# Performance work log

Hardware: AMD Instinct MI355X
Metric: run time of the kernel (lower is better)

The kernel has to match this reference:

```python
import jax, jax.numpy as jnp
import numpy as np


def _leaky(x):
    return jnp.where(x >= 0, x, 0.01 * x)  # nn.LeakyReLU default slope


def _conv1x1(x, w):
    # x: [B, C, H, W], w: [O, C] (1x1 conv == per-pixel channel GEMM)
    return jnp.einsum('bchw,oc->bohw', x, w)


def setup_inputs() -> dict:
    key = jax.random.key(0)
    ks = jax.random.split(key, 12)

    def kaiming(k, o, c):  # kaiming_normal_ fan_out, relu gain, 1x1 kernel
        return jax.random.normal(k, (o, c), jnp.float32) * np.float32(np.sqrt(2.0 / o))

    lr_feature = jax.random.normal(ks[0], (1, 32, 256, 512), jnp.float32)
    hr_feature = jax.random.normal(ks[1], (1, 32, 512, 1024), jnp.float32)
    return {
        'lr_feature': lr_feature,
        'hr_feature': hr_feature,
        's1_w0': kaiming(ks[2], 128, 128),
        's1_w1': kaiming(ks[3], 64, 128),
        's1_w2': kaiming(ks[4], 32, 64),
        's1_w3': kaiming(ks[5], 16, 32),
        's1_w4': kaiming(ks[6], 8, 16),
        's1_w5': kaiming(ks[7], 1, 8),
        's2_w0': kaiming(ks[8], 3, 3),
        's2_w1': kaiming(ks[9], 2, 3),
        's2_w2': kaiming(ks[10], 1, 2),
        'fuse_w': jnp.ones((1, 2), jnp.float32),  # fuse weight initialized to 1
    }


def reference(lr_feature, hr_feature, s1_w0, s1_w1, s1_w2, s1_w3, s1_w4, s1_w5,
              s2_w0, s2_w1, s2_w2, fuse_w):
    scale = hr_feature.shape[-1] // lr_feature.shape[-1]  # static python int (=2, even)
    Hh, Wh = hr_feature.shape[-2], hr_feature.shape[-1]

    # nearest-neighbor upsample of lr_feature by `scale` (expand/view trick in torch)
    lr_up = jnp.repeat(jnp.repeat(lr_feature, scale, axis=2), scale, axis=3)

    # representation: [B, 128, Hh, Wh]
    rep = jnp.concatenate(
        [lr_up, hr_feature, lr_up * hr_feature, (lr_up - hr_feature) ** 2], axis=1)

    # similarity_measure1: 1x1-conv MLP chain 128->128->64->32->16->8->1
    o = _leaky(_conv1x1(rep, s1_w0))
    o = _leaky(_conv1x1(o, s1_w1))
    o = _leaky(_conv1x1(o, s1_w2))
    o = _leaky(_conv1x1(o, s1_w3))
    o = _conv1x1(o, s1_w4)
    weights1 = _conv1x1(o, s1_w5)  # [B, 1, Hh, Wh]

    # distance matrix (even-scale branch): 3 channels [dx, dy, norm]
    v = jnp.arange(-(scale // 2), scale // 2 + 1, dtype=jnp.float32)
    m = v.shape[0] // 2
    v = jnp.concatenate([v[:m], v[m + 1:]])  # drop center -> length `scale`
    d0 = jnp.broadcast_to(v[None, :], (scale, scale))
    dm = jnp.stack([d0, d0.T, jnp.sqrt(d0 ** 2 + d0.T ** 2)], axis=0)  # [3,s,s]
    dm = jnp.tile(dm, (1, Hh // scale, Wh // scale))[None]  # [1, 3, Hh, Wh]

    # similarity_measure2: 3->3->2->1
    w2 = _leaky(_conv1x1(dm, s2_w0))
    w2 = _leaky(_conv1x1(w2, s2_w1))
    weights2 = _conv1x1(w2, s2_w2)  # [1, 1, Hh, Wh]

    # fuse (weight forced non-negative via abs, as in forward's .data mutation)
    mapping = _conv1x1(jnp.concatenate([weights1, weights2], axis=1), jnp.abs(fuse_w))
    return mapping
```

## Files before the change

kernel.cpp:

```cpp
#include <hip/hip_runtime.h>

typedef short v8s __attribute__((ext_vector_type(8)));
typedef float v4f __attribute__((ext_vector_type(4)));
typedef unsigned v4u __attribute__((ext_vector_type(4)));

#define Wh   1024
#define Hh   512
#define HWh  (Wh * Hh)
#define Wlr  512
#define HWlr (Wlr * 256)
#define ITERS 4
#define NBLK  512

#define WFRAG_SHORTS (53 * 512)
#define LDS_FRAGS    48
#define LDS_BYTES    (LDS_FRAGS * 1024)

__device__ __forceinline__ unsigned short f2bf(float f) {
    union { float f; unsigned u; } v; v.f = f;
    unsigned r = v.u + 0x7FFFu + ((v.u >> 16) & 1u);
    return (unsigned short)(r >> 16);
}
__device__ __forceinline__ unsigned pk2(float a, float b) {
    unsigned r;
    asm("v_cvt_pk_bf16_f32 %0, %1, %2" : "=v"(r) : "v"(a), "v"(b));
    return r;
}
__device__ __forceinline__ float leaky(float x) { return fmaxf(x, 0.01f * x); }

__device__ __forceinline__ v8s relay(v4f e, v4f o) {
    v4u w;
    w[0] = pk2(leaky(e[0]), leaky(e[1]));
    w[1] = pk2(leaky(e[2]), leaky(e[3]));
    w[2] = pk2(leaky(o[0]), leaky(o[1]));
    w[3] = pk2(leaky(o[2]), leaky(o[3]));
    return __builtin_bit_cast(v8s, w);
}

__global__ void prep_kernel(const float* __restrict__ w0g, const float* __restrict__ w1g,
                            const float* __restrict__ w2g, const float* __restrict__ w3g,
                            unsigned short* __restrict__ ws)
{
    const int f = blockIdx.x;
    const int l = threadIdx.x;
    const int pp = l & 15, qq = l >> 4;
    unsigned short* dst = ws + f * 512 + l * 8;

    if (f < 32) {
        int mt = f >> 2, ks = f & 3;
        const float* src = w0g + (mt * 16 + pp) * 128 + ks * 32 + qq * 8;
#pragma unroll
        for (int j = 0; j < 8; ++j) dst[j] = f2bf(src[j]);
    } else if (f < 48) {
        int g = f - 32, mt = g >> 2, ks = g & 3;
        const float* srcrow = w1g + (mt * 16 + pp) * 128;
#pragma unroll
        for (int j = 0; j < 8; ++j)
            dst[j] = f2bf(srcrow[ks * 32 + ((j >> 2) << 4) + qq * 4 + (j & 3)]);
    } else if (f < 52) {
        int g = f - 48, mt = g >> 1, ks = g & 1;
        const float* srcrow = w2g + (mt * 16 + pp) * 64;
#pragma unroll
        for (int j = 0; j < 8; ++j)
            dst[j] = f2bf(srcrow[ks * 32 + ((j >> 2) << 4) + qq * 4 + (j & 3)]);
    } else {
        const float* srcrow = w3g + pp * 32;
#pragma unroll
        for (int j = 0; j < 8; ++j)
            dst[j] = f2bf(srcrow[((j >> 2) << 4) + qq * 4 + (j & 3)]);
    }
}

__global__ __launch_bounds__(1024, 4)
void cmfsm_kernel(const float* __restrict__ lr, const float* __restrict__ hr,
                  const unsigned short* __restrict__ ws,
                  const float* __restrict__ w4g, const float* __restrict__ w5g,
                  const float* __restrict__ t0g, const float* __restrict__ t1g,
                  const float* __restrict__ t2g, const float* __restrict__ fwg,
                  float* __restrict__ out)
{
    extern __shared__ unsigned short smem[];
    unsigned short* wfrag = smem;

    const int tid  = threadIdx.x;
    const int lane = tid & 63;
    const int wv   = tid >> 6;
    const int p    = lane & 15;
    const int q    = lane >> 4;

    {
        const uint4* src = (const uint4*)ws;
        uint4* dst = (uint4*)smem;
#pragma unroll
        for (int e = 0; e < 3; ++e) dst[tid + e * 1024] = src[tid + e * 1024];
    }

    float w45[4];
#pragma unroll
    for (int r = 0; r < 4; ++r) {
        float s = 0.f;
#pragma unroll
        for (int j = 0; j < 8; ++j) s += w5g[j] * w4g[j * 16 + q * 4 + r];
        w45[r] = s;
    }

    const int row = blockIdx.x;

    float w2e, w2o;
    {
        float tab[4];
#pragma unroll
        for (int yp = 0; yp < 2; ++yp)
#pragma unroll
            for (int xp = 0; xp < 2; ++xp) {
                float i0 = xp ? 1.f : -1.f;
                float i1 = yp ? 1.f : -1.f;
                float i2 = 1.41421356237309505f;
                float h0[3], h1[2];
                for (int o = 0; o < 3; ++o)
                    h0[o] = leaky(t0g[o*3+0]*i0 + t0g[o*3+1]*i1 + t0g[o*3+2]*i2);
                for (int o = 0; o < 2; ++o)
                    h1[o] = leaky(t1g[o*3+0]*h0[0] + t1g[o*3+1]*h0[1] + t1g[o*3+2]*h0[2]);
                tab[yp*2+xp] = t2g[0]*h1[0] + t2g[1]*h1[1];
            }
        const int yp = row & 1;
        w2e = yp ? tab[2] : tab[0];
        w2o = yp ? tab[3] : tab[1];
    }
    const float fa = fabsf(fwg[0]);
    const float fb = fabsf(fwg[1]);

    const v8s a2w[4] = {
        *(const v8s*)(ws + 48 * 512 + lane * 8), *(const v8s*)(ws + 49 * 512 + lane * 8),
        *(const v8s*)(ws + 50 * 512 + lane * 8), *(const v8s*)(ws + 51 * 512 + lane * 8)
    };
    const v8s a3 = *(const v8s*)(ws + 52 * 512 + lane * 8);

    __syncthreads();

    const unsigned short* WL = wfrag + lane * 8;

    const float* hrp[8];
    const float* lrp[8];
    {
        const int hbase = row * Wh + wv * 16 + p;
        const int lbase = (row >> 1) * Wlr + wv * 8 + (p >> 1);
#pragma unroll
        for (int j = 0; j < 8; ++j) {
            hrp[j] = hr + (size_t)(q * 8 + j) * HWh  + hbase;
            lrp[j] = lr + (size_t)(q * 8 + j) * HWlr + lbase;
        }
    }

    const int obase = row * Wh + wv * 16 + p;

    float h[8], l[8];
#pragma unroll
    for (int j = 0; j < 8; ++j) { h[j] = hrp[j][0]; l[j] = lrp[j][0]; }

#pragma unroll
    for (int it = 0; it < ITERS; ++it) {
        v4u bf0, bf1, bf2, bf3;
#pragma unroll
        for (int u = 0; u < 4; ++u) {
            float l0 = l[2*u], l1 = l[2*u+1];
            float h0 = h[2*u], h1 = h[2*u+1];
            bf0[u] = pk2(l0, l1);
            bf1[u] = pk2(h0, h1);
            bf2[u] = pk2(l0 * h0, l1 * h1);
            float d0 = l0 - h0, d1 = l1 - h1;
            bf3[u] = pk2(d0 * d0, d1 * d1);
        }
        v8s b0 = __builtin_bit_cast(v8s, bf0);
        v8s b1 = __builtin_bit_cast(v8s, bf1);
        v8s b2 = __builtin_bit_cast(v8s, bf2);
        v8s b3 = __builtin_bit_cast(v8s, bf3);

        if (it + 1 < ITERS) {
            const int ho = (it + 1) * 256;
            const int lo = (it + 1) * 128;
#pragma unroll
            for (int j = 0; j < 8; ++j) {
                h[j] = hrp[j][ho];
                l[j] = lrp[j][lo];
            }
        }

        v8s c1[4];
#pragma unroll
        for (int ksp = 0; ksp < 4; ++ksp) {
            v4f ae = (v4f){0.f, 0.f, 0.f, 0.f};
            v4f ao = (v4f){0.f, 0.f, 0.f, 0.f};
#pragma unroll
            for (int ks = 0; ks < 4; ++ks) {
                v8s b = (ks == 0) ? b0 : (ks == 1) ? b1 : (ks == 2) ? b2 : b3;
                v8s we = *(const v8s*)(WL + ((2 * ksp)     * 4 + ks) * 512);
                v8s wo = *(const v8s*)(WL + ((2 * ksp + 1) * 4 + ks) * 512);
                ae = __builtin_amdgcn_mfma_f32_16x16x32_bf16(we, b, ae, 0, 0, 0);
                ao = __builtin_amdgcn_mfma_f32_16x16x32_bf16(wo, b, ao, 0, 0, 0);
            }
            c1[ksp] = relay(ae, ao);
        }

        v8s c2[2];
#pragma unroll
        for (int ksp = 0; ksp < 2; ++ksp) {
            v4f ae = (v4f){0.f, 0.f, 0.f, 0.f};
            v4f ao = (v4f){0.f, 0.f, 0.f, 0.f};
#pragma unroll
            for (int ks = 0; ks < 4; ++ks) {
                v8s we = *(const v8s*)(WL + (32 + (2 * ksp)     * 4 + ks) * 512);
                v8s wo = *(const v8s*)(WL + (32 + (2 * ksp + 1) * 4 + ks) * 512);
                ae = __builtin_amdgcn_mfma_f32_16x16x32_bf16(we, c1[ks], ae, 0, 0, 0);
                ao = __builtin_amdgcn_mfma_f32_16x16x32_bf16(wo, c1[ks], ao, 0, 0, 0);
            }
            c2[ksp] = relay(ae, ao);
        }

        v8s c3;
        {
            v4f ae = (v4f){0.f, 0.f, 0.f, 0.f};
            v4f ao = (v4f){0.f, 0.f, 0.f, 0.f};
#pragma unroll
            for (int ks = 0; ks < 2; ++ks) {
                ae = __builtin_amdgcn_mfma_f32_16x16x32_bf16(a2w[ks],     c2[ks], ae, 0, 0, 0);
                ao = __builtin_amdgcn_mfma_f32_16x16x32_bf16(a2w[2 + ks], c2[ks], ao, 0, 0, 0);
            }
            c3 = relay(ae, ao);
        }

        {
            v4f acc3 = __builtin_amdgcn_mfma_f32_16x16x32_bf16(a3, c3, (v4f){0.f, 0.f, 0.f, 0.f}, 0, 0, 0);

            float part = 0.f;
#pragma unroll
            for (int r = 0; r < 4; ++r) part += w45[r] * leaky(acc3[r]);
            part += __shfl_xor(part, 16, 64);
            part += __shfl_xor(part, 32, 64);

            if (q == 0) {
                const float w2v = (p & 1) ? w2o : w2e;
                out[obase + it * 256] = fa * part + fb * w2v;
            }
        }
    }
}

extern "C" void kernel_launch(void* const* d_in, const int* in_sizes, int n_in,
                              void* d_out, int out_size, void* d_ws, size_t ws_size,
                              hipStream_t stream) {
    const float* lr  = (const float*)d_in[0];
    const float* hr  = (const float*)d_in[1];
    const float* w0g = (const float*)d_in[2];
    const float* w1g = (const float*)d_in[3];
    const float* w2g = (const float*)d_in[4];
    const float* w3g = (const float*)d_in[5];
    const float* w4g = (const float*)d_in[6];
    const float* w5g = (const float*)d_in[7];
    const float* t0g = (const float*)d_in[8];
    const float* t1g = (const float*)d_in[9];
    const float* t2g = (const float*)d_in[10];
    const float* fwg = (const float*)d_in[11];
    float* out = (float*)d_out;
    unsigned short* ws = (unsigned short*)d_ws;

    hipLaunchKernelGGL(prep_kernel, dim3(53), dim3(64), 0, stream,
                       w0g, w1g, w2g, w3g, ws);
    hipLaunchKernelGGL(cmfsm_kernel, dim3(NBLK), dim3(1024), LDS_BYTES, stream,
                       lr, hr, ws, w4g, w5g, t0g, t1g, t2g, fwg, out);
}
```

Measured before the change: 144.7 us.

## Switch MLP chain from 16x16x32 to 32x32x16 bf16 MFMA tiles

Reworks the per-pixel MLP to use 32x32x16 MFMA instructions, so each wave handles 32 pixels with a 32-row output tile. Weight fragments are re-laid out in the prep kernel to the 32x32 operand format, and the last two small layers now also read from LDS instead of global memory. Blocks shrink to 512 threads with twice the pixels per wave. The goal is to cut LDS weight-fragment reads and per-tile overhead relative to the MFMA work, at the cost of more registers per thread and zero-padded work in the 16-output layer.

```diff
diff --git a/kernel.cpp b/kernel.cpp
--- a/kernel.cpp
+++ b/kernel.cpp
@@ -1,7 +1,7 @@
 #include <hip/hip_runtime.h>
 
 typedef short v8s __attribute__((ext_vector_type(8)));
-typedef float v4f __attribute__((ext_vector_type(4)));
+typedef float v16f __attribute__((ext_vector_type(16)));
 typedef unsigned v4u __attribute__((ext_vector_type(4)));
 
 #define Wh   1024
@@ -12,9 +12,8 @@
 #define ITERS 4
 #define NBLK  512
 
-#define WFRAG_SHORTS (53 * 512)
-#define LDS_FRAGS    48
-#define LDS_BYTES    (LDS_FRAGS * 1024)
+#define NFRAG     54
+#define LDS_BYTES (NFRAG * 1024)
 
 __device__ __forceinline__ unsigned short f2bf(float f) {
     union { float f; unsigned u; } v; v.f = f;
@@ -28,12 +27,20 @@
 }
 __device__ __forceinline__ float leaky(float x) { return fmaxf(x, 0.01f * x); }
 
-__device__ __forceinline__ v8s relay(v4f e, v4f o) {
+__device__ __forceinline__ v8s relayLo(const v16f& a) {
     v4u w;
-    w[0] = pk2(leaky(e[0]), leaky(e[1]));
-    w[1] = pk2(leaky(e[2]), leaky(e[3]));
-    w[2] = pk2(leaky(o[0]), leaky(o[1]));
-    w[3] = pk2(leaky(o[2]), leaky(o[3]));
+    w[0] = pk2(leaky(a[0]), leaky(a[1]));
+    w[1] = pk2(leaky(a[2]), leaky(a[3]));
+    w[2] = pk2(leaky(a[4]), leaky(a[5]));
+    w[3] = pk2(leaky(a[6]), leaky(a[7]));
+    return __builtin_bit_cast(v8s, w);
+}
+__device__ __forceinline__ v8s relayHi(const v16f& a) {
+    v4u w;
+    w[0] = pk2(leaky(a[8]),  leaky(a[9]));
+    w[1] = pk2(leaky(a[10]), leaky(a[11]));
+    w[2] = pk2(leaky(a[12]), leaky(a[13]));
+    w[3] = pk2(leaky(a[14]), leaky(a[15]));
     return __builtin_bit_cast(v8s, w);
 }
 
@@ -43,35 +50,37 @@
 {
     const int f = blockIdx.x;
     const int l = threadIdx.x;
-    const int pp = l & 15, qq = l >> 4;
+    const int r = l & 31, hi = l >> 5;
     unsigned short* dst = ws + f * 512 + l * 8;
 
     if (f < 32) {
-        int mt = f >> 2, ks = f & 3;
-        const float* src = w0g + (mt * 16 + pp) * 128 + ks * 32 + qq * 8;
+        int mt = f >> 3, t = f & 7;
+        const float* src = w0g + (mt * 32 + r) * 128 + t * 16 + hi * 8;
 #pragma unroll
         for (int j = 0; j < 8; ++j) dst[j] = f2bf(src[j]);
     } else if (f < 48) {
-        int g = f - 32, mt = g >> 2, ks = g & 3;
-        const float* srcrow = w1g + (mt * 16 + pp) * 128;
+        int g = f - 32, mt = g >> 3, t = g & 7;
+        const float* row = w1g + (mt * 32 + r) * 128;
 #pragma unroll
         for (int j = 0; j < 8; ++j)
-            dst[j] = f2bf(srcrow[ks * 32 + ((j >> 2) << 4) + qq * 4 + (j & 3)]);
+            dst[j] = f2bf(row[32 * (t >> 1) + 16 * (t & 1) + (j & 3) + 8 * (j >> 2) + 4 * hi]);
     } else if (f < 52) {
-        int g = f - 48, mt = g >> 1, ks = g & 1;
-        const float* srcrow = w2g + (mt * 16 + pp) * 64;
+        int t = f - 48;
+        const float* row = w2g + r * 64;
 #pragma unroll
         for (int j = 0; j < 8; ++j)
-            dst[j] = f2bf(srcrow[ks * 32 + ((j >> 2) << 4) + qq * 4 + (j & 3)]);
+            dst[j] = f2bf(row[32 * (t >> 1) + 16 * (t & 1) + (j & 3) + 8 * (j >> 2) + 4 * hi]);
     } else {
-        const float* srcrow = w3g + pp * 32;
+        int t = f - 52;
 #pragma unroll
         for (int j = 0; j < 8; ++j)
-            dst[j] = f2bf(srcrow[((j >> 2) << 4) + qq * 4 + (j & 3)]);
-    }
-}
-
-__global__ __launch_bounds__(1024, 4)
+            dst[j] = (r < 16)
+                ? f2bf(w3g[r * 32 + 16 * t + (j & 3) + 8 * (j >> 2) + 4 * hi])
+                : (unsigned short)0;
+    }
+}
+
+__global__ __launch_bounds__(512, 2)
 void cmfsm_kernel(const float* __restrict__ lr, const float* __restrict__ hr,
                   const unsigned short* __restrict__ ws,
                   const float* __restrict__ w4g, const float* __restrict__ w5g,
@@ -85,22 +94,26 @@
     const int tid  = threadIdx.x;
     const int lane = tid & 63;
     const int wv   = tid >> 6;
-    const int p    = lane & 15;
-    const int q    = lane >> 4;
+    const int n    = lane & 31;
+    const int hi   = lane >> 5;
 
     {
         const uint4* src = (const uint4*)ws;
         uint4* dst = (uint4*)smem;
 #pragma unroll
-        for (int e = 0; e < 3; ++e) dst[tid + e * 1024] = src[tid + e * 1024];
-    }
-
-    float w45[4];
-#pragma unroll
-    for (int r = 0; r < 4; ++r) {
+        for (int e = 0; e < 7; ++e) {
+            int idx = tid + e * 512;
+            if (idx < (NFRAG * 1024 / 16)) dst[idx] = src[idx];
+        }
+    }
+
+    float w45[8];
+#pragma unroll
+    for (int r = 0; r < 8; ++r) {
+        const int ch = (r & 3) + 8 * (r >> 2) + 4 * hi;
         float s = 0.f;
 #pragma unroll
-        for (int j = 0; j < 8; ++j) s += w5g[j] * w4g[j * 16 + q * 4 + r];
+        for (int j = 0; j < 8; ++j) s += w5g[j] * w4g[j * 16 + ch];
         w45[r] = s;
     }
 
@@ -130,116 +143,116 @@
     const float fa = fabsf(fwg[0]);
     const float fb = fabsf(fwg[1]);
 
-    const v8s a2w[4] = {
-        *(const v8s*)(ws + 48 * 512 + lane * 8), *(const v8s*)(ws + 49 * 512 + lane * 8),
-        *(const v8s*)(ws + 50 * 512 + lane * 8), *(const v8s*)(ws + 51 * 512 + lane * 8)
-    };
-    const v8s a3 = *(const v8s*)(ws + 52 * 512 + lane * 8);
-
     __syncthreads();
 
     const unsigned short* WL = wfrag + lane * 8;
 
-    const float* hrp[8];
-    const float* lrp[8];
+    const float* hrp[16];
+    const float* lrp[16];
     {
-        const int hbase = row * Wh + wv * 16 + p;
-        const int lbase = (row >> 1) * Wlr + wv * 8 + (p >> 1);
-#pragma unroll
-        for (int j = 0; j < 8; ++j) {
-            hrp[j] = hr + (size_t)(q * 8 + j) * HWh  + hbase;
-            lrp[j] = lr + (size_t)(q * 8 + j) * HWlr + lbase;
-        }
-    }
-
-    const int obase = row * Wh + wv * 16 + p;
-
-    float h[8], l[8];
-#pragma unroll
-    for (int j = 0; j < 8; ++j) { h[j] = hrp[j][0]; l[j] = lrp[j][0]; }
+        const int hbase = row * Wh + wv * 32 + n;
+        const int lbase = (row >> 1) * Wlr + wv * 16 + (n >> 1);
+#pragma unroll
+        for (int c = 0; c < 16; ++c) {
+            const int ch = (c < 8) ? (hi * 8 + c) : (16 + hi * 8 + (c - 8));
+            hrp[c] = hr + (size_t)ch * HWh  + hbase;
+            lrp[c] = lr + (size_t)ch * HWlr + lbase;
+        }
+    }
+
+    const int obase = row * Wh + wv * 32 + n;
+
+    const v16f z16 = (v16f){0.f,0.f,0.f,0.f,0.f,0.f,0.f,0.f,
+                            0.f,0.f,0.f,0.f,0.f,0.f,0.f,0.f};
+
+    float h[16], l[16];
+#pragma unroll
+    for (int c = 0; c < 16; ++c) { h[c] = hrp[c][0]; l[c] = lrp[c][0]; }
 
 #pragma unroll
     for (int it = 0; it < ITERS; ++it) {
-        v4u bf0, bf1, bf2, bf3;
+        v4u f0, f1, f2, f3, f4, f5, f6, f7;
 #pragma unroll
         for (int u = 0; u < 4; ++u) {
-            float l0 = l[2*u], l1 = l[2*u+1];
-            float h0 = h[2*u], h1 = h[2*u+1];
-            bf0[u] = pk2(l0, l1);
-            bf1[u] = pk2(h0, h1);
-            bf2[u] = pk2(l0 * h0, l1 * h1);
-            float d0 = l0 - h0, d1 = l1 - h1;
-            bf3[u] = pk2(d0 * d0, d1 * d1);
-        }
-        v8s b0 = __builtin_bit_cast(v8s, bf0);
-        v8s b1 = __builtin_bit_cast(v8s, bf1);
-        v8s b2 = __builtin_bit_cast(v8s, bf2);
-        v8s b3 = __builtin_bit_cast(v8s, bf3);
+            float la = l[2*u], lb = l[2*u+1], ha = h[2*u], hb = h[2*u+1];
+            float lA = l[8+2*u], lB = l[9+2*u], hA = h[8+2*u], hB = h[9+2*u];
+            f0[u] = pk2(la, lb);
+            f1[u] = pk2(lA, lB);
+            f2[u] = pk2(ha, hb);
+            f3[u] = pk2(hA, hB);
+            f4[u] = pk2(la * ha, lb * hb);
+            f5[u] = pk2(lA * hA, lB * hB);
+            float d0 = la - ha, d1 = lb - hb, D0 = lA - hA, D1 = lB - hB;
+            f6[u] = pk2(d0 * d0, d1 * d1);
+            f7[u] = pk2(D0 * D0, D1 * D1);
+        }
+        v8s b[8] = { __builtin_bit_cast(v8s, f0), __builtin_bit_cast(v8s, f1),
+                     __builtin_bit_cast(v8s, f2), __builtin_bit_cast(v8s, f3),
+                     __builtin_bit_cast(v8s, f4), __builtin_bit_cast(v8s, f5),
+                     __builtin_bit_cast(v8s, f6), __builtin_bit_cast(v8s, f7) };
 
         if (it + 1 < ITERS) {
             const int ho = (it + 1) * 256;
             const int lo = (it + 1) * 128;
 #pragma unroll
-            for (int j = 0; j < 8; ++j) {
-                h[j] = hrp[j][ho];
-                l[j] = lrp[j][lo];
-            }
-        }
-
-        v8s c1[4];
-#pragma unroll
-        for (int ksp = 0; ksp < 4; ++ksp) {
-            v4f ae = (v4f){0.f, 0.f, 0.f, 0.f};
-            v4f ao = (v4f){0.f, 0.f, 0.f, 0.f};
-#pragma unroll
-            for (int ks = 0; ks < 4; ++ks) {
-                v8s b = (ks == 0) ? b0 : (ks == 1) ? b1 : (ks == 2) ? b2 : b3;
-                v8s we = *(const v8s*)(WL + ((2 * ksp)     * 4 + ks) * 512);
-                v8s wo = *(const v8s*)(WL + ((2 * ksp + 1) * 4 + ks) * 512);
-                ae = __builtin_amdgcn_mfma_f32_16x16x32_bf16(we, b, ae, 0, 0, 0);
-                ao = __builtin_amdgcn_mfma_f32_16x16x32_bf16(wo, b, ao, 0, 0, 0);
-            }
-            c1[ksp] = relay(ae, ao);
-        }
-
-        v8s c2[2];
-#pragma unroll
-        for (int ksp = 0; ksp < 2; ++ksp) {
-            v4f ae = (v4f){0.f, 0.f, 0.f, 0.f};
-            v4f ao = (v4f){0.f, 0.f, 0.f, 0.f};
-#pragma unroll
-            for (int ks = 0; ks < 4; ++ks) {
-                v8s we = *(const v8s*)(WL + (32 + (2 * ksp)     * 4 + ks) * 512);
-                v8s wo = *(const v8s*)(WL + (32 + (2 * ksp + 1) * 4 + ks) * 512);
-                ae = __builtin_amdgcn_mfma_f32_16x16x32_bf16(we, c1[ks], ae, 0, 0, 0);
-                ao = __builtin_amdgcn_mfma_f32_16x16x32_bf16(wo, c1[ks], ao, 0, 0, 0);
-            }
-            c2[ksp] = relay(ae, ao);
-        }
-
-        v8s c3;
+            for (int c = 0; c < 16; ++c) {
+                h[c] = hrp[c][ho];
+                l[c] = lrp[c][lo];
+            }
+        }
+
+        v8s c1[8];
+#pragma unroll
+        for (int mt = 0; mt < 4; ++mt) {
+            v16f acc = z16;
+#pragma unroll
+            for (int t = 0; t < 8; ++t) {
+                v8s a = *(const v8s*)(WL + (mt * 8 + t) * 512);
+                acc = __builtin_amdgcn_mfma_f32_32x32x16_bf16(a, b[t], acc, 0, 0, 0);
+            }
+            c1[2 * mt]     = relayLo(acc);
+            c1[2 * mt + 1] = relayHi(acc);
+        }
+
+        v8s c2[4];
+#pragma unroll
+        for (int mt = 0; mt < 2; ++mt) {
+            v16f acc = z16;
+#pragma unroll
+            for (int t = 0; t < 8; ++t) {
+                v8s a = *(const v8s*)(WL + (32 + mt * 8 + t) * 512);
+                acc = __builtin_amdgcn_mfma_f32_32x32x16_bf16(a, c1[t], acc, 0, 0, 0);
+            }
+            c2[2 * mt]     = relayLo(acc);
+            c2[2 * mt + 1] = relayHi(acc);
+        }
+
+        v8s c3[2];
         {
-            v4f ae = (v4f){0.f, 0.f, 0.f, 0.f};
-            v4f ao = (v4f){0.f, 0.f, 0.f, 0.f};
-#pragma unroll
-            for (int ks = 0; ks < 2; ++ks) {
-                ae = __builtin_amdgcn_mfma_f32_16x16x32_bf16(a2w[ks],     c2[ks], ae, 0, 0, 0);
-                ao = __builtin_amdgcn_mfma_f32_16x16x32_bf16(a2w[2 + ks], c2[ks], ao, 0, 0, 0);
-            }
-            c3 = relay(ae, ao);
+            v16f acc = z16;
+#pragma unroll
+            for (int t = 0; t < 4; ++t) {
+                v8s a = *(const v8s*)(WL + (48 + t) * 512);
+                acc = __builtin_amdgcn_mfma_f32_32x32x16_bf16(a, c2[t], acc, 0, 0, 0);
+            }
+            c3[0] = relayLo(acc);
+            c3[1] = relayHi(acc);
         }
 
         {
-            v4f acc3 = __builtin_amdgcn_mfma_f32_16x16x32_bf16(a3, c3, (v4f){0.f, 0.f, 0.f, 0.f}, 0, 0, 0);
-
+            v16f acc = z16;
+#pragma unroll
+            for (int t = 0; t < 2; ++t) {
+                v8s a = *(const v8s*)(WL + (52 + t) * 512);
+                acc = __builtin_amdgcn_mfma_f32_32x32x16_bf16(a, c3[t], acc, 0, 0, 0);
+            }
             float part = 0.f;
 #pragma unroll
-            for (int r = 0; r < 4; ++r) part += w45[r] * leaky(acc3[r]);
-            part += __shfl_xor(part, 16, 64);
+            for (int r = 0; r < 8; ++r) part += w45[r] * leaky(acc[r]);
             part += __shfl_xor(part, 32, 64);
 
-            if (q == 0) {
-                const float w2v = (p & 1) ? w2o : w2e;
+            if (hi == 0) {
+                const float w2v = (n & 1) ? w2o : w2e;
                 out[obase + it * 256] = fa * part + fb * w2v;
             }
         }
@@ -264,8 +277,8 @@
     float* out = (float*)d_out;
     unsigned short* ws = (unsigned short*)d_ws;
 
-    hipLaunchKernelGGL(prep_kernel, dim3(53), dim3(64), 0, stream,
+    hipLaunchKernelGGL(prep_kernel, dim3(NFRAG), dim3(64), 0, stream,
                        w0g, w1g, w2g, w3g, ws);
-    hipLaunchKernelGGL(cmfsm_kernel, dim3(NBLK), dim3(1024), LDS_BYTES, stream,
+    hipLaunchKernelGGL(cmfsm_kernel, dim3(NBLK), dim3(512), LDS_BYTES, stream,
                        lr, hr, ws, w4g, w5g, t0g, t1g, t2g, fwg, out);
 }
```

Result: slower. 150.5 us (+4.0%).
